# Kernel tuning notes

Hardware: AMD Instinct MI355X
Metric: run time of the kernel (lower is better)

Reference implementation:

```python
import jax, jax.numpy as jnp
import numpy as np

N = 100000          # nodes
E = 1000000         # edges (before self loops)
F_IN = 128          # node feature dim
HEADS = [4, 2, 2]   # gat_heads
D = 48              # per-head out channels (hardcoded in module)
G = 64              # number of graphs in batch
FC_DIM = 192
OUT_DIM = 96
NEG_SLOPE = 0.2     # PyG GATConv default


def setup_inputs() -> dict:
    key = jax.random.key(0)
    ks = jax.random.split(key, 32)
    d = {
        "x": jax.random.normal(ks[0], (N, F_IN), jnp.float32),
        "edge_index": jax.random.randint(ks[1], (2, E), 0, N, dtype=jnp.int64),
        "batch": jnp.sort(jax.random.randint(ks[2], (N,), 0, G, dtype=jnp.int64)),
    }
    in_ch = F_IN
    k = 3
    for i, h in enumerate(HEADS):
        d[f"W{i}"] = jax.random.normal(ks[k], (in_ch, h * D), jnp.float32) / np.sqrt(in_ch); k += 1
        d[f"att_src{i}"] = jax.random.normal(ks[k], (h, D), jnp.float32) * 0.1; k += 1
        d[f"att_dst{i}"] = jax.random.normal(ks[k], (h, D), jnp.float32) * 0.1; k += 1
        d[f"bias{i}"] = jnp.zeros((h * D,), jnp.float32)
        in_ch = h * D
    d["fcW1"] = jax.random.normal(ks[k], (in_ch, FC_DIM), jnp.float32) / np.sqrt(in_ch); k += 1
    d["fcb1"] = jnp.zeros((FC_DIM,), jnp.float32)
    d["fcW2"] = jax.random.normal(ks[k], (FC_DIM, OUT_DIM), jnp.float32) / np.sqrt(FC_DIM); k += 1
    d["fcb2"] = jnp.zeros((OUT_DIM,), jnp.float32)
    return d


def _gat_layer(x, W, att_src, att_dst, bias, src, dst, heads):
    n = x.shape[0]
    h = (x @ W).reshape(n, heads, D)                    # [N,H,D]
    a_src = jnp.sum(h * att_src, axis=-1)               # [N,H]
    a_dst = jnp.sum(h * att_dst, axis=-1)               # [N,H]
    e = jax.nn.leaky_relu(a_src[src] + a_dst[dst], NEG_SLOPE)   # [Et,H]
    # segment softmax over incoming edges at each destination node
    m = jax.ops.segment_max(e, dst, num_segments=n)
    e = jnp.exp(e - m[dst])
    denom = jax.ops.segment_sum(e, dst, num_segments=n)
    alpha = e / (denom[dst] + 1e-16)                    # [Et,H]
    msg = h[src] * alpha[..., None]                     # [Et,H,D]
    out = jax.ops.segment_sum(msg, dst, num_segments=n) # [N,H,D]
    return out.reshape(n, heads * D) + bias


def reference(x, edge_index, batch,
              W0, att_src0, att_dst0, bias0,
              W1, att_src1, att_dst1, bias1,
              W2, att_src2, att_dst2, bias2,
              fcW1, fcb1, fcW2, fcb2):
    n = x.shape[0]
    loops = jnp.arange(n, dtype=edge_index.dtype)
    src = jnp.concatenate([edge_index[0], loops])   # add self loops (PyG default)
    dst = jnp.concatenate([edge_index[1], loops])
    x = jax.nn.relu(_gat_layer(x, W0, att_src0, att_dst0, bias0, src, dst, HEADS[0]))
    x = jax.nn.relu(_gat_layer(x, W1, att_src1, att_dst1, bias1, src, dst, HEADS[1]))
    x = jax.nn.relu(_gat_layer(x, W2, att_src2, att_dst2, bias2, src, dst, HEADS[2]))
    # global mean pool over graphs
    sums = jax.ops.segment_sum(x, batch, num_segments=G)
    counts = jax.ops.segment_sum(jnp.ones((n, 1), x.dtype), batch, num_segments=G)
    pooled = sums / jnp.maximum(counts, 1.0)
    h = jax.nn.relu(pooled @ fcW1 + fcb1)
    return h @ fcW2 + fcb2
```

## Files before the change

### kernel.cpp

```cpp
#include <hip/hip_runtime.h>

#define CAP 48
#define DD 48
#define BSH 8
#define NBUCK_MAX 400
#define CHUNK_MAX 4300

typedef short v8s __attribute__((ext_vector_type(8)));
typedef float v4f __attribute__((ext_vector_type(4)));
typedef float v2f __attribute__((ext_vector_type(2)));

__device__ __forceinline__ unsigned int bf16r(float f) {
    unsigned int u = __float_as_uint(f);
    return (u + 0x7FFFu + ((u >> 16) & 1u)) >> 16;
}

__device__ __forceinline__ v8s ld_frag(const ushort* p) {
    const uint2* q = reinterpret_cast<const uint2*>(p);
    uint2 a = q[0], b = q[1];
    union { unsigned int u[4]; v8s v; } t;
    t.u[0] = a.x; t.u[1] = a.y; t.u[2] = b.x; t.u[3] = b.y;
    return t.v;
}


__global__ void hist_kernel(const int* __restrict__ ei, int E, int N, int nbuck,
                            int* __restrict__ Hh) {
    __shared__ int lhist[NBUCK_MAX];
    int blk = blockIdx.x, t = threadIdx.x;
    int Et = E + N;
    int chunk = (Et + 255) >> 8;
    int lo = blk * chunk, hi = min(Et, lo + chunk);
    for (int i = t; i < nbuck; i += 256) lhist[i] = 0;
    __syncthreads();
    for (int e = lo + t; e < hi; e += 256) {
        int d = (e < E) ? ei[E + e] : (e - E);
        atomicAdd(&lhist[d >> BSH], 1);
    }
    __syncthreads();
    for (int b = t; b < nbuck; b += 256) Hh[b * 256 + blk] = lhist[b];
}

__global__ void scan_bucket_kernel(int* __restrict__ Hh, int* __restrict__ btot) {
    int b = blockIdx.x, lane = threadIdx.x;
    uint4 v = reinterpret_cast<uint4*>(Hh)[b * 64 + lane];
    unsigned s0 = v.x, s1 = s0 + v.y, s2 = s1 + v.z, s3 = s2 + v.w;
    unsigned incl = s3;
#pragma unroll
    for (int off = 1; off < 64; off <<= 1) {
        unsigned tmp = __shfl_up(incl, off);
        if (lane >= off) incl += tmp;
    }
    unsigned excl = incl - s3;
    reinterpret_cast<uint4*>(Hh)[b * 64 + lane] =
        make_uint4(excl, excl + s0, excl + s1, excl + s2);
    if (lane == 63) btot[b] = (int)incl;
}

__global__ void scan_base_kernel(const int* __restrict__ btot, int* __restrict__ bbase, int nbuck) {
    int lane = threadIdx.x;
    int carry = 0;
    int nch = (nbuck + 63) >> 6;
    for (int c = 0; c < nch; c++) {
        int idx = c * 64 + lane;
        int val = (idx < nbuck) ? btot[idx] : 0;
        int incl = val;
#pragma unroll
        for (int off = 1; off < 64; off <<= 1) {
            int tmp = __shfl_up(incl, off);
            if (lane >= off) incl += tmp;
        }
        if (idx < nbuck) bbase[idx] = carry + incl - val;
        carry += __shfl(incl, 63);
    }
    if (lane == 0) bbase[nbuck] = carry;
}

__global__ void add_base_kernel(int* __restrict__ Hh, const int* __restrict__ bbase) {
    Hh[blockIdx.x * 256 + threadIdx.x] += bbase[blockIdx.x];
}

__global__ void scatter_kernel(const int* __restrict__ ei, int E, int N, int nbuck,
                               const int* __restrict__ Hh, unsigned int* __restrict__ P) {
    __shared__ unsigned int sp[CHUNK_MAX];
    __shared__ int ga[CHUNK_MAX];
    __shared__ int lhist[NBUCK_MAX], lbaseL[NBUCK_MAX], lbaseG[NBUCK_MAX], lcur[NBUCK_MAX];
    int blk = blockIdx.x, t = threadIdx.x;
    int Et = E + N;
    int chunk = (Et + 255) >> 8;
    int lo = blk * chunk, hi = min(Et, lo + chunk);
    for (int i = t; i < nbuck; i += 256) { lhist[i] = 0; lcur[i] = 0; }
    __syncthreads();
    for (int e = lo + t; e < hi; e += 256) {
        int d = (e < E) ? ei[E + e] : (e - E);
        atomicAdd(&lhist[d >> BSH], 1);
    }
    __syncthreads();
    if (t < 64) {
        int lane = t, carry = 0;
        int nch = (nbuck + 63) >> 6;
        for (int c = 0; c < nch; c++) {
            int idx = c * 64 + lane;
            int val = (idx < nbuck) ? lhist[idx] : 0;
            int incl = val;
#pragma unroll
            for (int off = 1; off < 64; off <<= 1) {
                int tmp = __shfl_up(incl, off);
                if (lane >= off) incl += tmp;
            }
            if (idx < nbuck) {
                lbaseL[idx] = carry + incl - val;
                lbaseG[idx] = Hh[idx * 256 + blk];
            }
            carry += __shfl(incl, 63);
        }
    }
    __syncthreads();
    for (int e = lo + t; e < hi; e += 256) {
        int s, d;
        if (e < E) { s = ei[e]; d = ei[E + e]; } else { s = e - E; d = e - E; }
        int b = d >> BSH;
        int lpos = atomicAdd(&lcur[b], 1);
        int loc = lbaseL[b] + lpos;
        sp[loc] = ((unsigned)(d & 255) << 24) | (unsigned)s;
        ga[loc] = lbaseG[b] + lpos;
    }
    __syncthreads();
    int len = hi - lo;
    for (int i = t; i < len; i += 256) P[ga[i]] = sp[i];
}

__global__ void buildadj_kernel(const unsigned int* __restrict__ P, const int* __restrict__ bbase,
                                int* __restrict__ adj, int* __restrict__ cnt, int N) {
    __shared__ int slab[256 * CAP];
    __shared__ int cntL[256];
    int b = blockIdx.x, t = threadIdx.x;
    int n0 = b << BSH;
    int nodes = min(256, N - n0);
    cntL[t] = 0;
    __syncthreads();
    int lo = bbase[b], hi = bbase[b + 1];
    for (int i = lo + t; i < hi; i += 256) {
        unsigned p = P[i];
        int dloc = (int)(p >> 24);
        int s = (int)(p & 0x1FFFFu);
        int lpos = atomicAdd(&cntL[dloc], 1);
        if (lpos < CAP) slab[dloc * CAP + lpos] = s;
    }
    __syncthreads();
    int tot = nodes * CAP;
    for (int i = t; i < tot; i += 256) adj[(long)n0 * CAP + i] = slab[i];
    if (t < nodes) cnt[n0 + t] = min(cntL[t], CAP);
}

__global__ void cast_x_kernel(const float* __restrict__ x, unsigned int* __restrict__ xb, long n2) {
    long i = (long)blockIdx.x * blockDim.x + threadIdx.x;
    if (i >= n2) return;
    float2 v = reinterpret_cast<const float2*>(x)[i];
    xb[i] = bf16r(v.x) | (bf16r(v.y) << 16);
}

__global__ void convw_kernel(const float* __restrict__ W, ushort* __restrict__ WT, int K, int NC) {
    int i = blockIdx.x * blockDim.x + threadIdx.x;
    if (i >= K * NC) return;
    int k = i / NC, n = i % NC;
    WT[n * K + k] = (ushort)bf16r(W[i]);
}

template<int K, int NCT, int HEADS>
__global__ void gemm_mfma(const ushort* __restrict__ Xb, const ushort* __restrict__ WT,
                          const float* __restrict__ att_s, const float* __restrict__ att_d,
                          ushort* __restrict__ Hb, float* __restrict__ asrc,
                          float* __restrict__ adst, int N) {
    __shared__ ushort XT_l[128 * 40];
    __shared__ ushort WT_l[96 * 40];
    int tid = threadIdx.x;
    int wv = tid >> 6, lane = tid & 63;
    int m = lane & 15, quad = lane >> 4;
    int rb = blockIdx.x * 128;
    int c0 = blockIdx.y * 96;
    int mw = wv * 32;
    v4f acc[2][6];
#pragma unroll
    for (int mi = 0; mi < 2; mi++)
#pragma unroll
        for (int nb = 0; nb < 6; nb++) acc[mi][nb] = (v4f){0.f, 0.f, 0.f, 0.f};

    for (int k0 = 0; k0 < K; k0 += 32) {
#pragma unroll
        for (int t = 0; t < 2; t++) {
            int ch = tid + t * 256;
            int r = ch >> 2, kq = ch & 3;
            int rg = rb + r;
            uint4 v = make_uint4(0u, 0u, 0u, 0u);
            if (rg < N) v = *reinterpret_cast<const uint4*>(&Xb[(long)rg * K + k0 + kq * 8]);
            uint2* d = reinterpret_cast<uint2*>(&XT_l[r * 40 + kq * 8]);
            d[0] = make_uint2(v.x, v.y);
            d[1] = make_uint2(v.z, v.w);
        }
#pragma unroll
        for (int t = 0; t < 2; t++) {
            int ch = tid + t * 256;
            if (ch < 384) {
                int wr = ch >> 2, kq = ch & 3;
                uint4 v = *reinterpret_cast<const uint4*>(&WT[(long)(c0 + wr) * K + k0 + kq * 8]);
                uint2* d = reinterpret_cast<uint2*>(&WT_l[wr * 40 + kq * 8]);
                d[0] = make_uint2(v.x, v.y);
                d[1] = make_uint2(v.z, v.w);
            }
        }
        __syncthreads();
        v8s af[2], bf[6];
        af[0] = ld_frag(&XT_l[(mw + m) * 40 + quad * 8]);
        af[1] = ld_frag(&XT_l[(mw + 16 + m) * 40 + quad * 8]);
#pragma unroll
        for (int nb = 0; nb < 6; nb++)
            bf[nb] = ld_frag(&WT_l[(nb * 16 + m) * 40 + quad * 8]);
#pragma unroll
        for (int mi = 0; mi < 2; mi++)
#pragma unroll
            for (int nb = 0; nb < 6; nb++)
                acc[mi][nb] = __builtin_amdgcn_mfma_f32_16x16x32_bf16(af[mi], bf[nb], acc[mi][nb], 0, 0, 0);
        __syncthreads();
    }

#pragma unroll
    for (int mi = 0; mi < 2; mi++)
#pragma unroll
        for (int r = 0; r < 4; r++) {
            int R = rb + mw + mi * 16 + quad * 4 + r;
            if (R < N) {
#pragma unroll
                for (int nb = 0; nb < 6; nb++)
                    Hb[(long)R * NCT + c0 + nb * 16 + m] = (ushort)bf16r(acc[mi][nb][r]);
            }
        }

    float aS[6], aD[6];
    int h0 = c0 / DD;
#pragma unroll
    for (int nb = 0; nb < 6; nb++) {
        int cb = nb * 16 + m;
        int hl = cb / DD;
        int cih = cb - hl * DD;
        aS[nb] = att_s[(h0 + hl) * DD + cih];
        aD[nb] = att_d[(h0 + hl) * DD + cih];
    }
#pragma unroll
    for (int mi = 0; mi < 2; mi++)
#pragma unroll
        for (int r = 0; r < 4; r++) {
            float ps0 = 0.f, ps1 = 0.f, pd0 = 0.f, pd1 = 0.f;
#pragma unroll
            for (int nb = 0; nb < 3; nb++) {
                ps0 = fmaf(acc[mi][nb][r], aS[nb], ps0);
                pd0 = fmaf(acc[mi][nb][r], aD[nb], pd0);
            }
#pragma unroll
            for (int nb = 3; nb < 6; nb++) {
                ps1 = fmaf(acc[mi][nb][r], aS[nb], ps1);
                pd1 = fmaf(acc[mi][nb][r], aD[nb], pd1);
            }
#pragma unroll
            for (int d = 1; d < 16; d <<= 1) {
                ps0 += __shfl_xor(ps0, d); ps1 += __shfl_xor(ps1, d);
                pd0 += __shfl_xor(pd0, d); pd1 += __shfl_xor(pd1, d);
            }
            int R = rb + mw + mi * 16 + quad * 4 + r;
            if (m == 0 && R < N) {
                asrc[R * HEADS + h0]     = ps0;
                asrc[R * HEADS + h0 + 1] = ps1;
                adst[R * HEADS + h0]     = pd0;
                adst[R * HEADS + h0 + 1] = pd1;
            }
        }
}

template<int OUT, int HEADS, int EPW, bool OBF16>
__global__ void agg_kernel(const unsigned int* __restrict__ Hb,
                           const float* __restrict__ asrc, const float* __restrict__ adst,
                           const int* __restrict__ adj, const int* __restrict__ cnt,
                           const float* __restrict__ bias,
                           unsigned int* __restrict__ Ob, float* __restrict__ Of, int N) {
    constexpr int LPE = 64 / EPW;
    constexpr int ROWU = OUT / 2;
    __shared__ float wlds[4][HEADS][65];
    __shared__ float dlds[4][HEADS];
    __shared__ int   slds[4][64];
    int wv = threadIdx.x >> 6;
    int lane = threadIdx.x & 63;
    int esub = lane / LPE;
    int lp   = lane % LPE;
    int n = blockIdx.x * 4 + wv;
    bool valid = (n < N);
    int nn = valid ? n : 0;
    int deg_raw = cnt[nn];
    int araw = (lane < CAP) ? adj[(long)nn * CAP + lane] : 0;
    int deg = min(deg_raw, CAP);
    int s = (lane < deg) ? araw : 0;
    slds[wv][lane] = s;

    float av[HEADS], dvv[HEADS];
    if constexpr (HEADS == 4) {
        float4 t = *reinterpret_cast<const float4*>(&asrc[s * 4]);
        av[0] = t.x; av[1] = t.y; av[2] = t.z; av[3] = t.w;
        float4 u = *reinterpret_cast<const float4*>(&adst[nn * 4]);
        dvv[0] = u.x; dvv[1] = u.y; dvv[2] = u.z; dvv[3] = u.w;
    } else {
        float2 t = *reinterpret_cast<const float2*>(&asrc[s * 2]);
        av[0] = t.x; av[1] = t.y;
        float2 u = *reinterpret_cast<const float2*>(&adst[nn * 2]);
        dvv[0] = u.x; dvv[1] = u.y;
    }
    float w[HEADS];
#pragma unroll
    for (int h = 0; h < HEADS; h++) {
        float e = av[h] + dvv[h];
        e = (e < 0.f) ? 0.2f * e : e;
        w[h] = (lane < deg) ? __expf(e) : 0.f;
        wlds[wv][h][lane] = w[h];
    }
#pragma unroll
    for (int h = 0; h < HEADS; h++) {
        float dsum = w[h];
#pragma unroll
        for (int off = 1; off < 64; off <<= 1) dsum += __shfl_xor(dsum, off);
        if (lane == 0) dlds[wv][h] = dsum;
    }
    __syncthreads();

    int c = lp * 6;
    int head = c / DD;
    const float* wrow = &wlds[wv][head][0];
    v2f a0 = (v2f){0.f, 0.f}, a1 = (v2f){0.f, 0.f}, a2 = (v2f){0.f, 0.f};

    for (int base = 0; base < deg; base += 2 * EPW) {
        int e0 = base + esub, e1 = base + EPW + esub;
        int s0 = slds[wv][e0], s1 = slds[wv][e1];
        uint3 h0 = *reinterpret_cast<const uint3*>(&Hb[(long)s0 * ROWU + lp * 3]);
        uint3 h1 = *reinterpret_cast<const uint3*>(&Hb[(long)s1 * ROWU + lp * 3]);
        float w0 = wrow[e0], w1 = wrow[e1];
        v2f p;
        p.x = __uint_as_float(h0.x << 16); p.y = __uint_as_float(h0.x & 0xFFFF0000u);
        a0 += w0 * p;
        p.x = __uint_as_float(h0.y << 16); p.y = __uint_as_float(h0.y & 0xFFFF0000u);
        a1 += w0 * p;
        p.x = __uint_as_float(h0.z << 16); p.y = __uint_as_float(h0.z & 0xFFFF0000u);
        a2 += w0 * p;
        p.x = __uint_as_float(h1.x << 16); p.y = __uint_as_float(h1.x & 0xFFFF0000u);
        a0 += w1 * p;
        p.x = __uint_as_float(h1.y << 16); p.y = __uint_as_float(h1.y & 0xFFFF0000u);
        a1 += w1 * p;
        p.x = __uint_as_float(h1.z << 16); p.y = __uint_as_float(h1.z & 0xFFFF0000u);
        a2 += w1 * p;
    }

#pragma unroll
    for (int off = LPE; off < 64; off <<= 1) {
        a0.x += __shfl_xor(a0.x, off); a0.y += __shfl_xor(a0.y, off);
        a1.x += __shfl_xor(a1.x, off); a1.y += __shfl_xor(a1.y, off);
        a2.x += __shfl_xor(a2.x, off); a2.y += __shfl_xor(a2.y, off);
    }

    if (valid && esub == 0) {
        float invd = 1.f / (dlds[wv][head] + 1e-16f);
        float o[6];
        o[0] = fmaxf(fmaf(a0.x, invd, bias[c + 0]), 0.f);
        o[1] = fmaxf(fmaf(a0.y, invd, bias[c + 1]), 0.f);
        o[2] = fmaxf(fmaf(a1.x, invd, bias[c + 2]), 0.f);
        o[3] = fmaxf(fmaf(a1.y, invd, bias[c + 3]), 0.f);
        o[4] = fmaxf(fmaf(a2.x, invd, bias[c + 4]), 0.f);
        o[5] = fmaxf(fmaf(a2.y, invd, bias[c + 5]), 0.f);
        if (OBF16) {
            uint3 pk;
            pk.x = bf16r(o[0]) | (bf16r(o[1]) << 16);
            pk.y = bf16r(o[2]) | (bf16r(o[3]) << 16);
            pk.z = bf16r(o[4]) | (bf16r(o[5]) << 16);
            *reinterpret_cast<uint3*>(&Ob[(long)n * ROWU + lp * 3]) = pk;
        } else {
            float* dst = &Of[(long)n * OUT + c];
            *reinterpret_cast<float2*>(dst)     = make_float2(o[0], o[1]);
            *reinterpret_cast<float2*>(dst + 2) = make_float2(o[2], o[3]);
            *reinterpret_cast<float2*>(dst + 4) = make_float2(o[4], o[5]);
        }
    }
}

__global__ void pool_kernel(const float* __restrict__ O, const int* __restrict__ batch,
                            float* __restrict__ sums, float* __restrict__ counts, int N) {
    int grp = threadIdx.x >> 7;
    int c = threadIdx.x & 127;
    int n0 = (blockIdx.x * 4 + grp) * 64;
    if (n0 >= N) return;
    int nend = min(N, n0 + 64);
    bool act = (c < 96);
    float acc = 0.f; int cl = 0;
    int cur = batch[n0];
    int n = n0;
    for (; n + 4 <= nend; n += 4) {
        int g0 = batch[n], g1 = batch[n + 1], g2 = batch[n + 2], g3 = batch[n + 3];
        float v0 = 0.f, v1 = 0.f, v2 = 0.f, v3 = 0.f;
        if (act) {
            v0 = O[(long)n * 96 + c];       v1 = O[(long)(n + 1) * 96 + c];
            v2 = O[(long)(n + 2) * 96 + c]; v3 = O[(long)(n + 3) * 96 + c];
        }
#define POOL_STEP(g, v)                                                        \
        if ((g) != cur) {                                                      \
            if (act) atomicAdd(&sums[cur * 96 + c], acc);                      \
            if (c == 96) atomicAdd(&counts[cur], (float)cl);                   \
            acc = 0.f; cl = 0; cur = (g);                                      \
        }                                                                      \
        acc += (v); cl++;
        POOL_STEP(g0, v0) POOL_STEP(g1, v1) POOL_STEP(g2, v2) POOL_STEP(g3, v3)
    }
    for (; n < nend; n++) {
        int g = batch[n];
        float v = act ? O[(long)n * 96 + c] : 0.f;
        POOL_STEP(g, v)
    }
#undef POOL_STEP
    if (act) atomicAdd(&sums[cur * 96 + c], acc);
    if (c == 96) atomicAdd(&counts[cur], (float)cl);
}

__global__ void fc_kernel(const float* __restrict__ sums, const float* __restrict__ counts,
                          const float* __restrict__ W1, const float* __restrict__ b1,
                          const float* __restrict__ W2, const float* __restrict__ b2,
                          float* __restrict__ out) {
    __shared__ float p[96];
    __shared__ float h1[192];
    int g = blockIdx.x, tid = threadIdx.x;
    if (tid < 96) p[tid] = sums[g * 96 + tid] / fmaxf(counts[g], 1.0f);
    __syncthreads();
    float s = b1[tid];
    for (int c = 0; c < 96; c++) s = fmaf(p[c], W1[c * 192 + tid], s);
    h1[tid] = fmaxf(s, 0.f);
    __syncthreads();
    if (tid < 96) {
        float s2 = b2[tid];
        for (int j = 0; j < 192; j++) s2 = fmaf(h1[j], W2[j * 96 + tid], s2);
        out[g * 96 + tid] = s2;
    }
}

extern "C" void kernel_launch(void* const* d_in, const int* in_sizes, int n_in,
                              void* d_out, int out_size, void* d_ws, size_t ws_size,
                              hipStream_t stream) {
    const float* x     = (const float*)d_in[0];
    const int*   ei    = (const int*)d_in[1];
    const int*   batch = (const int*)d_in[2];
    const float* W0  = (const float*)d_in[3];
    const float* as0 = (const float*)d_in[4];
    const float* ad0 = (const float*)d_in[5];
    const float* b0  = (const float*)d_in[6];
    const float* W1  = (const float*)d_in[7];
    const float* as1 = (const float*)d_in[8];
    const float* ad1 = (const float*)d_in[9];
    const float* b1  = (const float*)d_in[10];
    const float* W2  = (const float*)d_in[11];
    const float* as2 = (const float*)d_in[12];
    const float* ad2 = (const float*)d_in[13];
    const float* b2  = (const float*)d_in[14];
    const float* fcW1 = (const float*)d_in[15];
    const float* fcb1 = (const float*)d_in[16];
    const float* fcW2 = (const float*)d_in[17];
    const float* fcb2 = (const float*)d_in[18];

    const int N = in_sizes[0] / 128;
    const int E = in_sizes[1] / 2;
    const int Et = E + N;
    const int nbuck = (N + 255) >> 8;

    char* ws = (char*)d_ws;
    unsigned int* Xb   = (unsigned int*)ws;
    unsigned int* Hb   = (unsigned int*)(ws + (size_t)N * 256);
    unsigned int* Ob   = (unsigned int*)(ws + (size_t)N * 640);
    float*        Obuf = (float*)(ws + (size_t)N * 1024);
    float*        ASRC = (float*)(ws + (size_t)N * 1408);
    float*        ADST = (float*)(ws + (size_t)N * 1424);
    int*          ADJ  = (int*)(ws + (size_t)N * 1440);
    int*          CNT  = (int*)(ws + (size_t)N * 1632);
    float*        SUMS = (float*)(ws + (size_t)N * 1636);
    float*        COUNTS = SUMS + 64 * 96;
    ushort*       WT0  = (ushort*)(COUNTS + 64);
    ushort*       WT1  = WT0 + 192 * 128;
    ushort*       WT2  = WT1 + 96 * 192;
    char*         tail = (char*)(WT2 + 96 * 96);
    int*          HIST = (int*)tail;
    int*          BTOT = (int*)(tail + NBUCK_MAX * 256 * 4);
    int*          BBASE = (int*)(tail + NBUCK_MAX * 256 * 4 + NBUCK_MAX * 4);
    unsigned int* P    = (unsigned int*)(tail + NBUCK_MAX * 260 * 4 + 64);

    hipMemsetAsync(SUMS, 0, (64 * 96 + 64) * 4, stream);

    hist_kernel<<<256, 256, 0, stream>>>(ei, E, N, nbuck, HIST);
    scan_bucket_kernel<<<nbuck, 64, 0, stream>>>(HIST, BTOT);
    scan_base_kernel<<<1, 64, 0, stream>>>(BTOT, BBASE, nbuck);
    add_base_kernel<<<nbuck, 256, 0, stream>>>(HIST, BBASE);
    scatter_kernel<<<256, 256, 0, stream>>>(ei, E, N, nbuck, HIST, P);
    buildadj_kernel<<<nbuck, 256, 0, stream>>>(P, BBASE, ADJ, CNT, N);

    long n2 = (long)N * 64;
    cast_x_kernel<<<(int)((n2 + 255) / 256), 256, 0, stream>>>(x, Xb, n2);
    convw_kernel<<<(128 * 192 + 255) / 256, 256, 0, stream>>>(W0, WT0, 128, 192);
    convw_kernel<<<(192 * 96 + 255) / 256, 256, 0, stream>>>(W1, WT1, 192, 96);
    convw_kernel<<<(96 * 96 + 255) / 256, 256, 0, stream>>>(W2, WT2, 96, 96);

    int gb = (N + 127) / 128;

    gemm_mfma<128, 192, 4><<<dim3(gb, 2), 256, 0, stream>>>((const ushort*)Xb, WT0, as0, ad0,
                                                            (ushort*)Hb, ASRC, ADST, N);
    agg_kernel<192, 4, 2, true><<<(N + 3) / 4, 256, 0, stream>>>(Hb, ASRC, ADST, ADJ, CNT, b0, Ob, nullptr, N);

    gemm_mfma<192, 96, 2><<<dim3(gb, 1), 256, 0, stream>>>((const ushort*)Ob, WT1, as1, ad1,
                                                           (ushort*)Hb, ASRC, ADST, N);
    agg_kernel<96, 2, 4, true><<<(N + 3) / 4, 256, 0, stream>>>(Hb, ASRC, ADST, ADJ, CNT, b1, Ob, nullptr, N);

    gemm_mfma<96, 96, 2><<<dim3(gb, 1), 256, 0, stream>>>((const ushort*)Ob, WT2, as2, ad2,
                                                          (ushort*)Hb, ASRC, ADST, N);
    agg_kernel<96, 2, 4, false><<<(N + 3) / 4, 256, 0, stream>>>(Hb, ASRC, ADST, ADJ, CNT, b2, nullptr, Obuf, N);

    pool_kernel<<<(N / 256) + 1, 512, 0, stream>>>(Obuf, batch, SUMS, COUNTS, N);
    fc_kernel<<<64, 192, 0, stream>>>(SUMS, COUNTS, fcW1, fcb1, fcW2, fcb2, (float*)d_out);
}
```

Measured before the change: 467.2 us.

## Software-pipeline the neighbor gather and widen per-lane chunks in the GAT aggregation

The aggregation kernel now gives each lane 12 output columns and doubles the edges handled per wave step (EPW 2→4 and 4→8). It also prefetches the next iteration's bf16 neighbor rows into registers before accumulating the current ones, to hide gather latency. The block-wide __syncthreads and the LDS denominator array are replaced by wave barriers, with per-head denominators kept in registers. The cost is higher register pressure from doubled accumulators and prefetch buffers, plus one extra, wasted prefetch at the end of the loop.

```diff
diff --git a/kernel.cpp b/kernel.cpp
--- a/kernel.cpp
+++ b/kernel.cpp
@@ -284,8 +284,8 @@
                            unsigned int* __restrict__ Ob, float* __restrict__ Of, int N) {
     constexpr int LPE = 64 / EPW;
     constexpr int ROWU = OUT / 2;
+    static_assert(LPE * 6 == ROWU, "lane chunk is 6 uints");
     __shared__ float wlds[4][HEADS][65];
-    __shared__ float dlds[4][HEADS];
     __shared__ int   slds[4][64];
     int wv = threadIdx.x >> 6;
     int lane = threadIdx.x & 63;
@@ -299,6 +299,22 @@
     int deg = min(deg_raw, CAP);
     int s = (lane < deg) ? araw : 0;
     slds[wv][lane] = s;
+    __builtin_amdgcn_wave_barrier();
+
+    int c = lp * 12;
+    int head = c / DD;
+
+    uint3 A0, A1, B0, B1;
+    {
+        int s0 = slds[wv][esub];
+        int s1 = slds[wv][EPW + esub];
+        const unsigned int* p0 = &Hb[(long)s0 * ROWU + lp * 6];
+        const unsigned int* p1 = &Hb[(long)s1 * ROWU + lp * 6];
+        A0 = *reinterpret_cast<const uint3*>(p0);
+        A1 = *reinterpret_cast<const uint3*>(p0 + 3);
+        B0 = *reinterpret_cast<const uint3*>(p1);
+        B1 = *reinterpret_cast<const uint3*>(p1 + 3);
+    }
 
     float av[HEADS], dvv[HEADS];
     if constexpr (HEADS == 4) {
@@ -312,7 +328,7 @@
         float2 u = *reinterpret_cast<const float2*>(&adst[nn * 2]);
         dvv[0] = u.x; dvv[1] = u.y;
     }
-    float w[HEADS];
+    float w[HEADS], den[HEADS];
 #pragma unroll
     for (int h = 0; h < HEADS; h++) {
         float e = av[h] + dvv[h];
@@ -325,34 +341,43 @@
         float dsum = w[h];
 #pragma unroll
         for (int off = 1; off < 64; off <<= 1) dsum += __shfl_xor(dsum, off);
-        if (lane == 0) dlds[wv][h] = dsum;
-    }
-    __syncthreads();
-
-    int c = lp * 6;
-    int head = c / DD;
+        den[h] = dsum;
+    }
+    __builtin_amdgcn_wave_barrier();
+
     const float* wrow = &wlds[wv][head][0];
     v2f a0 = (v2f){0.f, 0.f}, a1 = (v2f){0.f, 0.f}, a2 = (v2f){0.f, 0.f};
-
-    for (int base = 0; base < deg; base += 2 * EPW) {
-        int e0 = base + esub, e1 = base + EPW + esub;
-        int s0 = slds[wv][e0], s1 = slds[wv][e1];
-        uint3 h0 = *reinterpret_cast<const uint3*>(&Hb[(long)s0 * ROWU + lp * 3]);
-        uint3 h1 = *reinterpret_cast<const uint3*>(&Hb[(long)s1 * ROWU + lp * 3]);
-        float w0 = wrow[e0], w1 = wrow[e1];
+    v2f a3 = (v2f){0.f, 0.f}, a4 = (v2f){0.f, 0.f}, a5 = (v2f){0.f, 0.f};
+
+    auto ACC6 = [&](const uint3& lo, const uint3& hi, float wgt) {
         v2f p;
-        p.x = __uint_as_float(h0.x << 16); p.y = __uint_as_float(h0.x & 0xFFFF0000u);
-        a0 += w0 * p;
-        p.x = __uint_as_float(h0.y << 16); p.y = __uint_as_float(h0.y & 0xFFFF0000u);
-        a1 += w0 * p;
-        p.x = __uint_as_float(h0.z << 16); p.y = __uint_as_float(h0.z & 0xFFFF0000u);
-        a2 += w0 * p;
-        p.x = __uint_as_float(h1.x << 16); p.y = __uint_as_float(h1.x & 0xFFFF0000u);
-        a0 += w1 * p;
-        p.x = __uint_as_float(h1.y << 16); p.y = __uint_as_float(h1.y & 0xFFFF0000u);
-        a1 += w1 * p;
-        p.x = __uint_as_float(h1.z << 16); p.y = __uint_as_float(h1.z & 0xFFFF0000u);
-        a2 += w1 * p;
+        p.x = __uint_as_float(lo.x << 16); p.y = __uint_as_float(lo.x & 0xFFFF0000u); a0 += wgt * p;
+        p.x = __uint_as_float(lo.y << 16); p.y = __uint_as_float(lo.y & 0xFFFF0000u); a1 += wgt * p;
+        p.x = __uint_as_float(lo.z << 16); p.y = __uint_as_float(lo.z & 0xFFFF0000u); a2 += wgt * p;
+        p.x = __uint_as_float(hi.x << 16); p.y = __uint_as_float(hi.x & 0xFFFF0000u); a3 += wgt * p;
+        p.x = __uint_as_float(hi.y << 16); p.y = __uint_as_float(hi.y & 0xFFFF0000u); a4 += wgt * p;
+        p.x = __uint_as_float(hi.z << 16); p.y = __uint_as_float(hi.z & 0xFFFF0000u); a5 += wgt * p;
+    };
+
+    int nb = (deg + 2 * EPW - 1) / (2 * EPW);
+    for (int it = 0; it < nb; it++) {
+        int nbase = (it + 1) * 2 * EPW;
+        uint3 nA0, nA1, nB0, nB1;
+        {
+            int s0n = slds[wv][nbase + esub];
+            int s1n = slds[wv][nbase + EPW + esub];
+            const unsigned int* p0 = &Hb[(long)s0n * ROWU + lp * 6];
+            const unsigned int* p1 = &Hb[(long)s1n * ROWU + lp * 6];
+            nA0 = *reinterpret_cast<const uint3*>(p0);
+            nA1 = *reinterpret_cast<const uint3*>(p0 + 3);
+            nB0 = *reinterpret_cast<const uint3*>(p1);
+            nB1 = *reinterpret_cast<const uint3*>(p1 + 3);
+        }
+        int e0 = it * 2 * EPW + esub;
+        float w0 = wrow[e0], w1 = wrow[e0 + EPW];
+        ACC6(A0, A1, w0);
+        ACC6(B0, B1, w1);
+        A0 = nA0; A1 = nA1; B0 = nB0; B1 = nB1;
     }
 
 #pragma unroll
@@ -360,28 +385,48 @@
         a0.x += __shfl_xor(a0.x, off); a0.y += __shfl_xor(a0.y, off);
         a1.x += __shfl_xor(a1.x, off); a1.y += __shfl_xor(a1.y, off);
         a2.x += __shfl_xor(a2.x, off); a2.y += __shfl_xor(a2.y, off);
+        a3.x += __shfl_xor(a3.x, off); a3.y += __shfl_xor(a3.y, off);
+        a4.x += __shfl_xor(a4.x, off); a4.y += __shfl_xor(a4.y, off);
+        a5.x += __shfl_xor(a5.x, off); a5.y += __shfl_xor(a5.y, off);
     }
 
     if (valid && esub == 0) {
-        float invd = 1.f / (dlds[wv][head] + 1e-16f);
-        float o[6];
-        o[0] = fmaxf(fmaf(a0.x, invd, bias[c + 0]), 0.f);
-        o[1] = fmaxf(fmaf(a0.y, invd, bias[c + 1]), 0.f);
-        o[2] = fmaxf(fmaf(a1.x, invd, bias[c + 2]), 0.f);
-        o[3] = fmaxf(fmaf(a1.y, invd, bias[c + 3]), 0.f);
-        o[4] = fmaxf(fmaf(a2.x, invd, bias[c + 4]), 0.f);
-        o[5] = fmaxf(fmaf(a2.y, invd, bias[c + 5]), 0.f);
+        float denh;
+        if constexpr (HEADS == 4) {
+            denh = (head == 0) ? den[0] : (head == 1) ? den[1] : (head == 2) ? den[2] : den[3];
+        } else {
+            denh = (head == 0) ? den[0] : den[1];
+        }
+        float invd = 1.f / (denh + 1e-16f);
+        float o[12];
+        o[0]  = fmaxf(fmaf(a0.x, invd, bias[c + 0]), 0.f);
+        o[1]  = fmaxf(fmaf(a0.y, invd, bias[c + 1]), 0.f);
+        o[2]  = fmaxf(fmaf(a1.x, invd, bias[c + 2]), 0.f);
+        o[3]  = fmaxf(fmaf(a1.y, invd, bias[c + 3]), 0.f);
+        o[4]  = fmaxf(fmaf(a2.x, invd, bias[c + 4]), 0.f);
+        o[5]  = fmaxf(fmaf(a2.y, invd, bias[c + 5]), 0.f);
+        o[6]  = fmaxf(fmaf(a3.x, invd, bias[c + 6]), 0.f);
+        o[7]  = fmaxf(fmaf(a3.y, invd, bias[c + 7]), 0.f);
+        o[8]  = fmaxf(fmaf(a4.x, invd, bias[c + 8]), 0.f);
+        o[9]  = fmaxf(fmaf(a4.y, invd, bias[c + 9]), 0.f);
+        o[10] = fmaxf(fmaf(a5.x, invd, bias[c + 10]), 0.f);
+        o[11] = fmaxf(fmaf(a5.y, invd, bias[c + 11]), 0.f);
         if (OBF16) {
-            uint3 pk;
-            pk.x = bf16r(o[0]) | (bf16r(o[1]) << 16);
-            pk.y = bf16r(o[2]) | (bf16r(o[3]) << 16);
-            pk.z = bf16r(o[4]) | (bf16r(o[5]) << 16);
-            *reinterpret_cast<uint3*>(&Ob[(long)n * ROWU + lp * 3]) = pk;
+            uint3 pk1, pk2;
+            pk1.x = bf16r(o[0])  | (bf16r(o[1])  << 16);
+            pk1.y = bf16r(o[2])  | (bf16r(o[3])  << 16);
+            pk1.z = bf16r(o[4])  | (bf16r(o[5])  << 16);
+            pk2.x = bf16r(o[6])  | (bf16r(o[7])  << 16);
+            pk2.y = bf16r(o[8])  | (bf16r(o[9])  << 16);
+            pk2.z = bf16r(o[10]) | (bf16r(o[11]) << 16);
+            unsigned int* dst = &Ob[(long)n * ROWU + lp * 6];
+            *reinterpret_cast<uint3*>(dst)     = pk1;
+            *reinterpret_cast<uint3*>(dst + 3) = pk2;
         } else {
             float* dst = &Of[(long)n * OUT + c];
-            *reinterpret_cast<float2*>(dst)     = make_float2(o[0], o[1]);
-            *reinterpret_cast<float2*>(dst + 2) = make_float2(o[2], o[3]);
-            *reinterpret_cast<float2*>(dst + 4) = make_float2(o[4], o[5]);
+            *reinterpret_cast<float4*>(dst)     = make_float4(o[0], o[1], o[2],  o[3]);
+            *reinterpret_cast<float4*>(dst + 4) = make_float4(o[4], o[5], o[6],  o[7]);
+            *reinterpret_cast<float4*>(dst + 8) = make_float4(o[8], o[9], o[10], o[11]);
         }
     }
 }
@@ -510,15 +555,15 @@
 
     gemm_mfma<128, 192, 4><<<dim3(gb, 2), 256, 0, stream>>>((const ushort*)Xb, WT0, as0, ad0,
                                                             (ushort*)Hb, ASRC, ADST, N);
-    agg_kernel<192, 4, 2, true><<<(N + 3) / 4, 256, 0, stream>>>(Hb, ASRC, ADST, ADJ, CNT, b0, Ob, nullptr, N);
+    agg_kernel<192, 4, 4, true><<<(N + 3) / 4, 256, 0, stream>>>(Hb, ASRC, ADST, ADJ, CNT, b0, Ob, nullptr, N);
 
     gemm_mfma<192, 96, 2><<<dim3(gb, 1), 256, 0, stream>>>((const ushort*)Ob, WT1, as1, ad1,
                                                            (ushort*)Hb, ASRC, ADST, N);
-    agg_kernel<96, 2, 4, true><<<(N + 3) / 4, 256, 0, stream>>>(Hb, ASRC, ADST, ADJ, CNT, b1, Ob, nullptr, N);
+    agg_kernel<96, 2, 8, true><<<(N + 3) / 4, 256, 0, stream>>>(Hb, ASRC, ADST, ADJ, CNT, b1, Ob, nullptr, N);
 
     gemm_mfma<96, 96, 2><<<dim3(gb, 1), 256, 0, stream>>>((const ushort*)Ob, WT2, as2, ad2,
                                                           (ushort*)Hb, ASRC, ADST, N);
-    agg_kernel<96, 2, 4, false><<<(N + 3) / 4, 256, 0, stream>>>(Hb, ASRC, ADST, ADJ, CNT, b2, nullptr, Obuf, N);
+    agg_kernel<96, 2, 8, false><<<(N + 3) / 4, 256, 0, stream>>>(Hb, ASRC, ADST, ADJ, CNT, b2, nullptr, Obuf, N);
 
     pool_kernel<<<(N / 256) + 1, 512, 0, stream>>>(Obuf, batch, SUMS, COUNTS, N);
     fc_kernel<<<64, 192, 0, stream>>>(SUMS, COUNTS, fcW1, fcb1, fcW2, fcb2, (float*)d_out);
```

New measurement: 472.7 us. Within noise of the previous version (+1.2%).
